# Performance work log

Hardware: AMD Instinct MI355X
Metric: run time of the kernel (lower is better)

Reference implementation:

```python
import jax, jax.numpy as jnp
import numpy as np

NUM_GRAPHS = 512  # number of distinct graph ids in batch


def _gcn_agg(x, batch):
    # mm(block_full_adj, x) == per-graph sum broadcast back to nodes
    sums = jax.ops.segment_sum(x, batch, num_segments=NUM_GRAPHS)
    return sums[batch]


def setup_inputs() -> dict:
    key = jax.random.key(0)
    ks = jax.random.split(key, 8)
    N, D = 100000, 128
    H = 2 * D
    x = jax.random.normal(ks[0], (N, D), dtype=jnp.float32)
    batch = jnp.sort(jax.random.randint(ks[1], (N,), 0, NUM_GRAPHS)).astype(jnp.int64)
    s = 0.05
    W1 = jax.random.normal(ks[2], (D, H), dtype=jnp.float32) * s
    b1 = jax.random.normal(ks[3], (H,), dtype=jnp.float32) * s
    W2 = jax.random.normal(ks[4], (H, H), dtype=jnp.float32) * s
    b2 = jax.random.normal(ks[5], (H,), dtype=jnp.float32) * s
    Wc = jax.random.normal(ks[6], (H, 1), dtype=jnp.float32) * s
    bc = jax.random.normal(ks[7], (1,), dtype=jnp.float32) * s
    return {"x": x, "batch": batch, "W1": W1, "b1": b1, "W2": W2, "b2": b2, "Wc": Wc, "bc": bc}


def reference(x, batch, W1, b1, W2, b2, Wc, bc):
    h = jax.nn.relu(_gcn_agg(x, batch) @ W1 + b1)          # GCN layer 1
    h = jax.nn.relu(_gcn_agg(h, batch) @ W2 + b2)          # GCN layer 2
    c = h @ Wc + bc                                         # confidence head
    sp = jax.nn.softplus(c)
    return sp / (1.0 + sp)
```

## Files before the change

### kernel.cpp

```cpp
#include <hip/hip_runtime.h>
#include <math.h>

#define NUM_GRAPHS 512
#define D 128
#define HDIM 256
#define K 4
#define GPB 4

#define DETECT_IS64(batch32, N, tid, sWave, sIs64)                         \
    {                                                                      \
        int cap = (N) < 1024 ? (N) : 1024;                                 \
        int local = 0x7fffffff;                                            \
        for (int i = (tid); i < cap; i += 256)                             \
            if ((batch32)[i] != 0) { local = i; break; }                   \
        for (int off = 32; off > 0; off >>= 1)                             \
            local = min(local, __shfl_down(local, off, 64));               \
        if (((tid) & 63) == 0) (sWave)[(tid) >> 6] = local;                \
        __syncthreads();                                                   \
        if ((tid) == 0) {                                                  \
            int j = min(min((sWave)[0], (sWave)[1]),                       \
                        min((sWave)[2], (sWave)[3]));                      \
            (sIs64) = (j != 0x7fffffff && j + 1 < (N) &&                   \
                       (batch32)[j + 1] == 0) ? 1 : 0;                     \
        }                                                                  \
        __syncthreads();                                                   \
    }

__device__ __forceinline__ int lower_bound_g(const int* batch32, int is64,
                                             int N, int target)
{
    const long long* batch64 = (const long long*)batch32;
    int lo = 0, hi = N;
    while (lo < hi) {
        int m = (lo + hi) >> 1;
        long long v = is64 ? batch64[m] : (long long)batch32[m];
        if (v < (long long)target) lo = m + 1; else hi = m;
    }
    return lo;
}

__global__ __launch_bounds__(256) void seg_sum(
    const float* __restrict__ x, const int* __restrict__ batch32,
    float4* __restrict__ partial4, int N)
{
    const int blk = blockIdx.x;
    const int g   = blk / K;
    const int k   = blk % K;
    const int tid = threadIdx.x;

    __shared__ int    sIs64;
    __shared__ int    sWave[4];
    __shared__ int    sStart, sEnd;
    __shared__ float4 part[256];

    DETECT_IS64(batch32, N, tid, sWave, sIs64);
    const int is64 = sIs64;

    if (tid < 2) {
        int lo = lower_bound_g(batch32, is64, N, g + tid);
        if (tid == 0) sStart = lo; else sEnd = lo;
    }
    __syncthreads();

    const int start = sStart, end = sEnd;
    const int n   = end - start;
    const int per = (n + K - 1) / K;
    const int r0  = start + k * per;
    const int r1  = min(r0 + per, end);

    const int r  = tid >> 5;
    const int c4 = tid & 31;
    float4 acc = make_float4(0.f, 0.f, 0.f, 0.f);
    const float4* x4 = (const float4*)x;
    for (int row = r0 + r; row < r1; row += 8) {
        float4 v = x4[row * 32 + c4];
        acc.x += v.x; acc.y += v.y; acc.z += v.z; acc.w += v.w;
    }
    part[tid] = acc;
    __syncthreads();
    for (int s = 4; s >= 1; s >>= 1) {
        if (r < s) {
            float4 o = part[tid + s * 32];
            float4 m = part[tid];
            m.x += o.x; m.y += o.y; m.z += o.z; m.w += o.w;
            part[tid] = m;
        }
        __syncthreads();
    }
    if (tid < 32)
        partial4[blk * 32 + tid] = part[tid];
}

__global__ __launch_bounds__(256) void mlp_scatter(
    const float* __restrict__ partial, const int* __restrict__ batch32,
    const float* __restrict__ W1, const float* __restrict__ b1,
    const float* __restrict__ W2, const float* __restrict__ b2,
    const float* __restrict__ Wc, const float* __restrict__ bc,
    float* __restrict__ out, int N)
{
    const int g0  = blockIdx.x * GPB;
    const int tid = threadIdx.x;

    __shared__ int   sIs64;
    __shared__ int   sWave[4];
    __shared__ int   sBound[GPB + 1];
    __shared__ float sS[GPB][D];
    __shared__ float sH[GPB][HDIM];
    __shared__ float sRed[4][GPB];
    __shared__ float sCval[GPB];

    DETECT_IS64(batch32, N, tid, sWave, sIs64);
    const int is64 = sIs64;

    if (tid <= GPB)
        sBound[tid] = lower_bound_g(batch32, is64, N, g0 + tid);
    __syncthreads();

    if (tid < D) {
        #pragma unroll
        for (int j = 0; j < GPB; ++j) {
            float s = 0.f;
            #pragma unroll
            for (int k = 0; k < K; ++k)
                s += partial[((g0 + j) * K + k) * D + tid];
            sS[j][tid] = s;
        }
    }
    __syncthreads();

    float a1[GPB];
    {
        float bb = b1[tid];
        #pragma unroll
        for (int j = 0; j < GPB; ++j) a1[j] = bb;
    }
    for (int k = 0; k < D; ++k) {
        float w = W1[k * HDIM + tid];
        #pragma unroll
        for (int j = 0; j < GPB; ++j) a1[j] = fmaf(sS[j][k], w, a1[j]);
    }
    #pragma unroll
    for (int j = 0; j < GPB; ++j) {
        float cnt = (float)(sBound[j + 1] - sBound[j]);
        sH[j][tid] = fmaxf(a1[j], 0.f) * cnt;
    }
    __syncthreads();

    float a2[GPB];
    {
        float bb = b2[tid];
        #pragma unroll
        for (int j = 0; j < GPB; ++j) a2[j] = bb;
    }
    for (int k = 0; k < HDIM; ++k) {
        float w = W2[k * HDIM + tid];
        #pragma unroll
        for (int j = 0; j < GPB; ++j) a2[j] = fmaf(sH[j][k], w, a2[j]);
    }
    float wc = Wc[tid];
    float v[GPB];
    #pragma unroll
    for (int j = 0; j < GPB; ++j) v[j] = fmaxf(a2[j], 0.f) * wc;
    for (int off = 32; off > 0; off >>= 1) {
        #pragma unroll
        for (int j = 0; j < GPB; ++j) v[j] += __shfl_down(v[j], off, 64);
    }
    if ((tid & 63) == 0) {
        #pragma unroll
        for (int j = 0; j < GPB; ++j) sRed[tid >> 6][j] = v[j];
    }
    __syncthreads();
    if (tid < GPB) {
        float cc = sRed[0][tid] + sRed[1][tid] + sRed[2][tid] + sRed[3][tid]
                 + bc[0];
        float m  = fmaxf(cc, 0.f);
        float sp = m + log1pf(expf(-fabsf(cc)));
        sCval[tid] = sp / (1.f + sp);
    }
    __syncthreads();

    #pragma unroll
    for (int j = 0; j < GPB; ++j) {
        float val = sCval[j];
        for (int i = sBound[j] + tid; i < sBound[j + 1]; i += 256)
            out[i] = val;
    }
}

extern "C" void kernel_launch(void* const* d_in, const int* in_sizes, int n_in,
                              void* d_out, int out_size, void* d_ws, size_t ws_size,
                              hipStream_t stream)
{
    const float* x   = (const float*)d_in[0];
    const int*   bat = (const int*)d_in[1];
    const float* W1  = (const float*)d_in[2];
    const float* b1  = (const float*)d_in[3];
    const float* W2  = (const float*)d_in[4];
    const float* b2  = (const float*)d_in[5];
    const float* Wc  = (const float*)d_in[6];
    const float* bc  = (const float*)d_in[7];
    float* out = (float*)d_out;
    const int N = in_sizes[0] / D;

    float* partial = (float*)d_ws;

    seg_sum<<<NUM_GRAPHS * K, 256, 0, stream>>>(x, bat, (float4*)partial, N);
    mlp_scatter<<<NUM_GRAPHS / GPB, 256, 0, stream>>>(partial, bat,
                                                      W1, b1, W2, b2, Wc, bc,
                                                      out, N);
}
```

Measured before the change: 126.1 us.

## Precompute segment bounds in a scan kernel and rebalance seg-sum and MLP grids

```diff
diff --git a/kernel.cpp b/kernel.cpp
--- a/kernel.cpp
+++ b/kernel.cpp
@@ -4,8 +4,10 @@
 #define NUM_GRAPHS 512
 #define D 128
 #define HDIM 256
-#define K 4
-#define GPB 4
+#define K 8
+#define GPB 2
+#define B0 64
+
 
 #define DETECT_IS64(batch32, N, tid, sWave, sIs64)                         \
     {                                                                      \
@@ -26,43 +28,49 @@
         __syncthreads();                                                   \
     }
 
-__device__ __forceinline__ int lower_bound_g(const int* batch32, int is64,
-                                             int N, int target)
-{
-    const long long* batch64 = (const long long*)batch32;
-    int lo = 0, hi = N;
-    while (lo < hi) {
-        int m = (lo + hi) >> 1;
-        long long v = is64 ? batch64[m] : (long long)batch32[m];
-        if (v < (long long)target) lo = m + 1; else hi = m;
-    }
-    return lo;
-}
-
-__global__ __launch_bounds__(256) void seg_sum(
-    const float* __restrict__ x, const int* __restrict__ batch32,
-    float4* __restrict__ partial4, int N)
-{
-    const int blk = blockIdx.x;
-    const int g   = blk / K;
-    const int k   = blk % K;
+__global__ __launch_bounds__(256) void bounds_scan(
+    const int* __restrict__ batch32, int* __restrict__ bounds, int N)
+{
     const int tid = threadIdx.x;
-
-    __shared__ int    sIs64;
-    __shared__ int    sWave[4];
-    __shared__ int    sStart, sEnd;
-    __shared__ float4 part[256];
-
+    __shared__ int sIs64;
+    __shared__ int sWave[4];
     DETECT_IS64(batch32, N, tid, sWave, sIs64);
     const int is64 = sIs64;
-
-    if (tid < 2) {
-        int lo = lower_bound_g(batch32, is64, N, g + tid);
-        if (tid == 0) sStart = lo; else sEnd = lo;
-    }
-    __syncthreads();
-
-    const int start = sStart, end = sEnd;
+    const long long* batch64 = (const long long*)batch32;
+
+    const int threads = B0 * 256;
+    const int per = (N + threads - 1) / threads;
+    const int gt  = blockIdx.x * 256 + tid;
+    const int i0  = gt * per;
+    const int i1  = min(i0 + per, N);
+
+    for (int i = i0; i < i1; ++i) {
+        int b = is64 ? (int)batch64[i] : batch32[i];
+        if (i == 0) {
+            for (int t = 0; t <= b; ++t) bounds[t] = 0;
+        } else {
+            int a = is64 ? (int)batch64[i - 1] : batch32[i - 1];
+            for (int t = a + 1; t <= b; ++t) bounds[t] = i;
+        }
+        if (i == N - 1) {
+            for (int t = b + 1; t <= NUM_GRAPHS; ++t) bounds[t] = N;
+        }
+    }
+}
+
+__global__ __launch_bounds__(256) void seg_sum(
+    const float* __restrict__ x, const int* __restrict__ bounds,
+    float4* __restrict__ partial4)
+{
+    const int blk = blockIdx.x;
+    const int g   = blk >> 3;
+    const int k   = blk & 7;
+    const int tid = threadIdx.x;
+
+    __shared__ float4 part[256];
+
+    const int start = bounds[g];
+    const int end   = bounds[g + 1];
     const int n   = end - start;
     const int per = (n + K - 1) / K;
     const int r0  = start + k * per;
@@ -92,39 +100,31 @@
 }
 
 __global__ __launch_bounds__(256) void mlp_scatter(
-    const float* __restrict__ partial, const int* __restrict__ batch32,
+    const float* __restrict__ partial, const int* __restrict__ bounds,
     const float* __restrict__ W1, const float* __restrict__ b1,
     const float* __restrict__ W2, const float* __restrict__ b2,
     const float* __restrict__ Wc, const float* __restrict__ bc,
-    float* __restrict__ out, int N)
+    float* __restrict__ out)
 {
     const int g0  = blockIdx.x * GPB;
     const int tid = threadIdx.x;
 
-    __shared__ int   sIs64;
-    __shared__ int   sWave[4];
     __shared__ int   sBound[GPB + 1];
     __shared__ float sS[GPB][D];
     __shared__ float sH[GPB][HDIM];
     __shared__ float sRed[4][GPB];
     __shared__ float sCval[GPB];
 
-    DETECT_IS64(batch32, N, tid, sWave, sIs64);
-    const int is64 = sIs64;
-
-    if (tid <= GPB)
-        sBound[tid] = lower_bound_g(batch32, is64, N, g0 + tid);
-    __syncthreads();
-
-    if (tid < D) {
-        #pragma unroll
-        for (int j = 0; j < GPB; ++j) {
-            float s = 0.f;
-            #pragma unroll
-            for (int k = 0; k < K; ++k)
-                s += partial[((g0 + j) * K + k) * D + tid];
-            sS[j][tid] = s;
-        }
+    if (tid <= GPB) sBound[tid] = bounds[g0 + tid];
+
+    {
+        const int j = tid >> 7;
+        const int dcol = tid & (D - 1);
+        float s = 0.f;
+        #pragma unroll
+        for (int k = 0; k < K; ++k)
+            s += partial[((g0 + j) * K + k) * D + dcol];
+        sS[j][dcol] = s;
     }
     __syncthreads();
 
@@ -134,6 +134,7 @@
         #pragma unroll
         for (int j = 0; j < GPB; ++j) a1[j] = bb;
     }
+    #pragma unroll 16
     for (int k = 0; k < D; ++k) {
         float w = W1[k * HDIM + tid];
         #pragma unroll
@@ -152,6 +153,7 @@
         #pragma unroll
         for (int j = 0; j < GPB; ++j) a2[j] = bb;
     }
+    #pragma unroll 16
     for (int k = 0; k < HDIM; ++k) {
         float w = W2[k * HDIM + tid];
         #pragma unroll
@@ -179,11 +181,11 @@
     }
     __syncthreads();
 
-    #pragma unroll
-    for (int j = 0; j < GPB; ++j) {
-        float val = sCval[j];
-        for (int i = sBound[j] + tid; i < sBound[j + 1]; i += 256)
-            out[i] = val;
+    {
+        const int s0 = sBound[0], s1 = sBound[1], s2 = sBound[GPB];
+        const float v0 = sCval[0], v1 = sCval[1];
+        for (int i = s0 + tid; i < s2; i += 256)
+            out[i] = (i < s1) ? v0 : v1;
     }
 }
 
@@ -202,10 +204,12 @@
     float* out = (float*)d_out;
     const int N = in_sizes[0] / D;
 
-    float* partial = (float*)d_ws;
-
-    seg_sum<<<NUM_GRAPHS * K, 256, 0, stream>>>(x, bat, (float4*)partial, N);
-    mlp_scatter<<<NUM_GRAPHS / GPB, 256, 0, stream>>>(partial, bat,
+    int*   bounds  = (int*)d_ws;
+    float* partial = (float*)((char*)d_ws + 4096);
+
+    bounds_scan<<<B0, 256, 0, stream>>>(bat, bounds, N);
+    seg_sum<<<NUM_GRAPHS * K, 256, 0, stream>>>(x, bounds, (float4*)partial);
+    mlp_scatter<<<NUM_GRAPHS / GPB, 256, 0, stream>>>(partial, bounds,
                                                       W1, b1, W2, b2, Wc, bc,
-                                                      out, N);
-}
+                                                      out);
+}
```

After: 113.2 us. 1.11x faster.
